# Kernel tuning notes

Hardware: AMD Instinct MI355X
Metric: run time of the kernel (lower is better)

Reference implementation:

```python
import jax, jax.numpy as jnp
import numpy as np

POOL = (2, 2)
STRIDES = (2, 2)


def _maxpool2d(x):
    # NHWC max pooling, VALID padding (matches K.pool2d(..., pool_mode='max'))
    return jax.lax.reduce_window(
        x, -jnp.inf, jax.lax.max,
        window_dimensions=(1, POOL[0], POOL[1], 1),
        window_strides=(1, STRIDES[0], STRIDES[1], 1),
        padding='VALID')


def setup_inputs() -> dict:
    key = jax.random.key(0)
    ks = jax.random.split(key, 8)
    B, H, W, C = 2, 64, 64, 128
    n_out = 32
    n_pool = (H // POOL[0]) * (W // POOL[1]) * C  # 131072
    y = jax.random.normal(ks[0], (B, H, W, C), jnp.float32)
    x_0 = jax.random.normal(ks[1], (B, 16), jnp.float32)
    mid = jax.random.normal(ks[2], (B, H, W, C), jnp.float32)
    rad = jax.random.uniform(ks[3], (B, H, W, C), jnp.float32)
    u_c = mid + rad  # valid interval bounds: l_c <= u_c
    l_c = mid - rad
    w_out_u = jax.random.normal(ks[4], (B, 1, n_pool, n_out), jnp.float32)
    b_out_u = jax.random.normal(ks[5], (B, 1, n_out), jnp.float32)
    w_out_l = jax.random.normal(ks[6], (B, 1, n_pool, n_out), jnp.float32)
    b_out_l = jax.random.normal(ks[7], (B, 1, n_out), jnp.float32)
    return {"y": y, "x_0": x_0, "u_c": u_c, "l_c": l_c,
            "w_out_u": w_out_u, "b_out_u": b_out_u,
            "w_out_l": w_out_l, "b_out_l": b_out_l}


def reference(y, x_0, u_c, l_c, w_out_u, b_out_u, w_out_l, b_out_l):
    # BackwardMaxPooling2D._pooling_function_fast, mode=F_IBP
    B = y.shape[0]
    # b_u_, b_l_: (B, 1, n_pool, 1) constant post-pool bounds
    b_u = _maxpool2d(u_c).reshape(B, 1, -1, 1)
    b_l = _maxpool2d(l_c).reshape(B, 1, -1, 1)
    n_in = int(np.prod(y.shape[1:]))
    n_out = w_out_u.shape[-1]
    # w_out_u_ = concat([0 * flatten(y)] * n_out) -> identically zero weights
    w_zero = jnp.broadcast_to(0.0 * y.reshape(B, 1, n_in, 1), (B, 1, n_in, n_out))
    # fold backward weights into constant biases using interval bounds
    b_out_u_ = (jnp.sum(jnp.maximum(w_out_u, 0.0) * b_u, axis=2)
                + jnp.sum(jnp.minimum(w_out_u, 0.0) * b_l, axis=2)
                + b_out_u)
    b_out_l_ = (jnp.sum(jnp.maximum(w_out_l, 0.0) * b_l, axis=2)
                + jnp.sum(jnp.minimum(w_out_l, 0.0) * b_u, axis=2)
                + b_out_l)
    return (w_zero, b_out_u_, w_zero, b_out_l_)
```

## Files before the change

### kernel.cpp

```cpp
#include <hip/hip_runtime.h>

#define BATCH 2
#define HH 64
#define WW 64
#define CC 128
#define OHH 32
#define OWW 32
#define NPOOL (OHH * OWW * CC)
#define NOUT 32
#define NIN (HH * WW * CC)
#define WZERO ((size_t)BATCH * NIN * NOUT)

#define OFF_BU (WZERO)
#define OFF_BL (2 * WZERO + (size_t)BATCH * NOUT)

#define CHUNKS 1024
#define PPC (NPOOL / CHUNKS)

__global__ void zero_kernel(float4* __restrict__ out, size_t n4) {
    size_t tid = (size_t)blockIdx.x * blockDim.x + threadIdx.x;
    size_t stride = (size_t)gridDim.x * blockDim.x;
    const float4 z = make_float4(0.f, 0.f, 0.f, 0.f);
    for (size_t i = tid; i < n4; i += stride)
        out[i] = z;
}

__global__ void pool_kernel(const float4* __restrict__ u_c,
                            const float4* __restrict__ l_c,
                            float4* __restrict__ bu,
                            float4* __restrict__ bl,
                            const float* __restrict__ b_out_u,
                            const float* __restrict__ b_out_l,
                            float* __restrict__ out) {
    int tid = blockIdx.x * blockDim.x + threadIdx.x;
    int c4 = tid & 31;
    int ow = (tid >> 5) & 31;
    int oh = (tid >> 10) & 31;
    int b  = tid >> 15;

    int base = ((b * HH + 2 * oh) * WW + 2 * ow) * (CC / 4) + c4;
    const int colstep = CC / 4;
    const int rowstep = WW * (CC / 4);

    {
        float4 a0 = u_c[base];
        float4 a1 = u_c[base + colstep];
        float4 a2 = u_c[base + rowstep];
        float4 a3 = u_c[base + rowstep + colstep];
        float4 m;
        m.x = fmaxf(fmaxf(a0.x, a1.x), fmaxf(a2.x, a3.x));
        m.y = fmaxf(fmaxf(a0.y, a1.y), fmaxf(a2.y, a3.y));
        m.z = fmaxf(fmaxf(a0.z, a1.z), fmaxf(a2.z, a3.z));
        m.w = fmaxf(fmaxf(a0.w, a1.w), fmaxf(a2.w, a3.w));
        bu[tid] = m;
    }
    {
        float4 a0 = l_c[base];
        float4 a1 = l_c[base + colstep];
        float4 a2 = l_c[base + rowstep];
        float4 a3 = l_c[base + rowstep + colstep];
        float4 m;
        m.x = fmaxf(fmaxf(a0.x, a1.x), fmaxf(a2.x, a3.x));
        m.y = fmaxf(fmaxf(a0.y, a1.y), fmaxf(a2.y, a3.y));
        m.z = fmaxf(fmaxf(a0.z, a1.z), fmaxf(a2.z, a3.z));
        m.w = fmaxf(fmaxf(a0.w, a1.w), fmaxf(a2.w, a3.w));
        bl[tid] = m;
    }

    if (blockIdx.x == 0 && threadIdx.x < BATCH * NOUT) {
        out[OFF_BU + threadIdx.x] = b_out_u[threadIdx.x];
        out[OFF_BL + threadIdx.x] = b_out_l[threadIdx.x];
    }
}

__global__ void reduce_kernel(const float4* __restrict__ wu,
                              const float4* __restrict__ wl,
                              const float* __restrict__ bu,
                              const float* __restrict__ bl,
                              float* __restrict__ out) {
    int b = blockIdx.x / CHUNKS;
    int chunk = blockIdx.x % CHUNKS;
    int t = threadIdx.x;
    int og = t & 7;
    int pl = t >> 3;

    float4 au = make_float4(0.f, 0.f, 0.f, 0.f);
    float4 al = make_float4(0.f, 0.f, 0.f, 0.f);

    const float* bub = bu + b * NPOOL;
    const float* blb = bl + b * NPOOL;
    int p0 = chunk * PPC;

#pragma unroll
    for (int it = 0; it < PPC / 32; ++it) {
        int p = p0 + pl + it * 32;
        float vbu = bub[p];
        float vbl = blb[p];
        size_t widx = ((size_t)b * NPOOL + p) * (NOUT / 4) + og;
        float4 u4 = wu[widx];
        float4 l4 = wl[widx];
        au.x += fmaxf(u4.x, 0.f) * vbu + fminf(u4.x, 0.f) * vbl;
        au.y += fmaxf(u4.y, 0.f) * vbu + fminf(u4.y, 0.f) * vbl;
        au.z += fmaxf(u4.z, 0.f) * vbu + fminf(u4.z, 0.f) * vbl;
        au.w += fmaxf(u4.w, 0.f) * vbu + fminf(u4.w, 0.f) * vbl;
        al.x += fmaxf(l4.x, 0.f) * vbl + fminf(l4.x, 0.f) * vbu;
        al.y += fmaxf(l4.y, 0.f) * vbl + fminf(l4.y, 0.f) * vbu;
        al.z += fmaxf(l4.z, 0.f) * vbl + fminf(l4.z, 0.f) * vbu;
        al.w += fmaxf(l4.w, 0.f) * vbl + fminf(l4.w, 0.f) * vbu;
    }

    __shared__ float4 su[256];
    __shared__ float4 sl[256];
    su[t] = au;
    sl[t] = al;
    __syncthreads();

    for (int s = 128; s >= 8; s >>= 1) {
        if (t < s) {
            float4 xu = su[t + s];
            su[t].x += xu.x; su[t].y += xu.y; su[t].z += xu.z; su[t].w += xu.w;
            float4 xl = sl[t + s];
            sl[t].x += xl.x; sl[t].y += xl.y; sl[t].z += xl.z; sl[t].w += xl.w;
        }
        __syncthreads();
    }

    if (t < 8) {
        float4 ru = su[t];
        float4 rl = sl[t];
        float* ou = out + OFF_BU + (size_t)b * NOUT + t * 4;
        float* ol = out + OFF_BL + (size_t)b * NOUT + t * 4;
        atomicAdd(&ou[0], ru.x);
        atomicAdd(&ou[1], ru.y);
        atomicAdd(&ou[2], ru.z);
        atomicAdd(&ou[3], ru.w);
        atomicAdd(&ol[0], rl.x);
        atomicAdd(&ol[1], rl.y);
        atomicAdd(&ol[2], rl.z);
        atomicAdd(&ol[3], rl.w);
    }
}

extern "C" void kernel_launch(void* const* d_in, const int* in_sizes, int n_in,
                              void* d_out, int out_size, void* d_ws, size_t ws_size,
                              hipStream_t stream) {
    const float* u_c     = (const float*)d_in[2];
    const float* l_c     = (const float*)d_in[3];
    const float* w_out_u = (const float*)d_in[4];
    const float* b_out_u = (const float*)d_in[5];
    const float* w_out_l = (const float*)d_in[6];
    const float* b_out_l = (const float*)d_in[7];
    float* out = (float*)d_out;

    float* ws_bu = (float*)d_ws;
    float* ws_bl = ws_bu + (size_t)BATCH * NPOOL;

    size_t n4 = (size_t)out_size / 4;
    zero_kernel<<<2048, 256, 0, stream>>>((float4*)out, n4);

    pool_kernel<<<256, 256, 0, stream>>>(
        (const float4*)u_c, (const float4*)l_c,
        (float4*)ws_bu, (float4*)ws_bl,
        b_out_u, b_out_l, out);

    reduce_kernel<<<BATCH * CHUNKS, 256, 0, stream>>>(
        (const float4*)w_out_u, (const float4*)w_out_l,
        ws_bu, ws_bl, out);
}
```

Measured before the change: 418.9 us.

## Use nontemporal stores/loads and replace atomics with partial-sum final reduction

The zero-fill of the large weight output now uses nontemporal stores with a larger grid. The streaming weight loads in the reduce kernel become nontemporal loads. The per-block atomicAdd accumulation is replaced by writing per-chunk partial sums to workspace, followed by a single-block final kernel that sums them and adds the biases. This removes atomic contention and cache pollution, at the cost of an extra serial launch whose one block loops over 1024 partials.

Result: faster. 367.5 us (-12.3%).

```diff
diff --git a/kernel.cpp b/kernel.cpp
--- a/kernel.cpp
+++ b/kernel.cpp
@@ -17,21 +17,20 @@
 #define CHUNKS 1024
 #define PPC (NPOOL / CHUNKS)
 
-__global__ void zero_kernel(float4* __restrict__ out, size_t n4) {
+typedef float vfloat4 __attribute__((ext_vector_type(4)));
+
+__global__ void zero_kernel(vfloat4* __restrict__ out, size_t n4) {
     size_t tid = (size_t)blockIdx.x * blockDim.x + threadIdx.x;
     size_t stride = (size_t)gridDim.x * blockDim.x;
-    const float4 z = make_float4(0.f, 0.f, 0.f, 0.f);
+    const vfloat4 z = {0.f, 0.f, 0.f, 0.f};
     for (size_t i = tid; i < n4; i += stride)
-        out[i] = z;
+        __builtin_nontemporal_store(z, &out[i]);
 }
 
 __global__ void pool_kernel(const float4* __restrict__ u_c,
                             const float4* __restrict__ l_c,
                             float4* __restrict__ bu,
-                            float4* __restrict__ bl,
-                            const float* __restrict__ b_out_u,
-                            const float* __restrict__ b_out_l,
-                            float* __restrict__ out) {
+                            float4* __restrict__ bl) {
     int tid = blockIdx.x * blockDim.x + threadIdx.x;
     int c4 = tid & 31;
     int ow = (tid >> 5) & 31;
@@ -66,18 +65,13 @@
         m.w = fmaxf(fmaxf(a0.w, a1.w), fmaxf(a2.w, a3.w));
         bl[tid] = m;
     }
-
-    if (blockIdx.x == 0 && threadIdx.x < BATCH * NOUT) {
-        out[OFF_BU + threadIdx.x] = b_out_u[threadIdx.x];
-        out[OFF_BL + threadIdx.x] = b_out_l[threadIdx.x];
-    }
 }
 
-__global__ void reduce_kernel(const float4* __restrict__ wu,
-                              const float4* __restrict__ wl,
+__global__ void reduce_kernel(const vfloat4* __restrict__ wu,
+                              const vfloat4* __restrict__ wl,
                               const float* __restrict__ bu,
                               const float* __restrict__ bl,
-                              float* __restrict__ out) {
+                              float4* __restrict__ part) {
     int b = blockIdx.x / CHUNKS;
     int chunk = blockIdx.x % CHUNKS;
     int t = threadIdx.x;
@@ -97,8 +91,8 @@
         float vbu = bub[p];
         float vbl = blb[p];
         size_t widx = ((size_t)b * NPOOL + p) * (NOUT / 4) + og;
-        float4 u4 = wu[widx];
-        float4 l4 = wl[widx];
+        vfloat4 u4 = __builtin_nontemporal_load(&wu[widx]);
+        vfloat4 l4 = __builtin_nontemporal_load(&wl[widx]);
         au.x += fmaxf(u4.x, 0.f) * vbu + fminf(u4.x, 0.f) * vbl;
         au.y += fmaxf(u4.y, 0.f) * vbu + fminf(u4.y, 0.f) * vbl;
         au.z += fmaxf(u4.z, 0.f) * vbu + fminf(u4.z, 0.f) * vbl;
@@ -126,18 +120,30 @@
     }
 
     if (t < 8) {
-        float4 ru = su[t];
-        float4 rl = sl[t];
-        float* ou = out + OFF_BU + (size_t)b * NOUT + t * 4;
-        float* ol = out + OFF_BL + (size_t)b * NOUT + t * 4;
-        atomicAdd(&ou[0], ru.x);
-        atomicAdd(&ou[1], ru.y);
-        atomicAdd(&ou[2], ru.z);
-        atomicAdd(&ou[3], ru.w);
-        atomicAdd(&ol[0], rl.x);
-        atomicAdd(&ol[1], rl.y);
-        atomicAdd(&ol[2], rl.z);
-        atomicAdd(&ol[3], rl.w);
+        size_t row = ((size_t)b * CHUNKS + chunk) * 16;
+        part[row + t] = su[t];
+        part[row + 8 + t] = sl[t];
+    }
+}
+
+__global__ void final_kernel(const float* __restrict__ part,
+                             const float* __restrict__ b_out_u,
+                             const float* __restrict__ b_out_l,
+                             float* __restrict__ out) {
+    int j = threadIdx.x;
+    int b = j >> 6;
+    int slot = j & 63;
+
+    float acc = 0.f;
+    const float* p = part + (size_t)b * CHUNKS * 64 + slot;
+    for (int c = 0; c < CHUNKS; ++c)
+        acc += p[(size_t)c * 64];
+
+    if (slot < 32) {
+        out[OFF_BU + b * NOUT + slot] = acc + b_out_u[b * NOUT + slot];
+    } else {
+        int o = slot - 32;
+        out[OFF_BL + b * NOUT + o] = acc + b_out_l[b * NOUT + o];
     }
 }
 
@@ -154,16 +160,18 @@
 
     float* ws_bu = (float*)d_ws;
     float* ws_bl = ws_bu + (size_t)BATCH * NPOOL;
+    float* ws_part = ws_bl + (size_t)BATCH * NPOOL;
 
     size_t n4 = (size_t)out_size / 4;
-    zero_kernel<<<2048, 256, 0, stream>>>((float4*)out, n4);
+    zero_kernel<<<4096, 256, 0, stream>>>((vfloat4*)out, n4);
 
     pool_kernel<<<256, 256, 0, stream>>>(
         (const float4*)u_c, (const float4*)l_c,
-        (float4*)ws_bu, (float4*)ws_bl,
-        b_out_u, b_out_l, out);
+        (float4*)ws_bu, (float4*)ws_bl);
 
     reduce_kernel<<<BATCH * CHUNKS, 256, 0, stream>>>(
-        (const float4*)w_out_u, (const float4*)w_out_l,
-        ws_bu, ws_bl, out);
+        (const vfloat4*)w_out_u, (const vfloat4*)w_out_l,
+        ws_bu, ws_bl, (float4*)ws_part);
+
+    final_kernel<<<1, 128, 0, stream>>>(ws_part, b_out_u, b_out_l, out);
 }
```
